# Performance work log

Hardware: AMD Instinct MI355X
Metric: run time of the kernel (lower is better)

## Reference

```python
import jax, jax.numpy as jnp
import numpy as np

ALPHA = 0.2  # LeakyReLU negative slope
NEG_BIG = -9e15


def setup_inputs() -> dict:
    key = jax.random.key(0)
    k1, k2, k3, k4 = jax.random.split(key, 4)
    N, F_IN, F_OUT = 8192, 256, 128
    h = jax.random.normal(k1, (N, F_IN), dtype=jnp.float32)
    adj = jax.random.randint(k2, (N, N), 0, 2, dtype=jnp.int32)
    # xavier_uniform with gain=1.414
    def xavier(k, shape, gain=1.414):
        fan_in, fan_out = shape[0], shape[1]
        bound = gain * np.sqrt(6.0 / (fan_in + fan_out))
        return jax.random.uniform(k, shape, jnp.float32, -bound, bound)
    W = xavier(k3, (F_IN, F_OUT))
    a = xavier(k4, (2 * F_OUT, 1))
    return {"h": h, "adj": adj, "W": W, "a": a}


def reference(h, adj, W, a):
    # Wh: [N, F_out]
    Wh = h @ W
    F_out = W.shape[1]
    a1 = a[:F_out, 0]   # attends to source (row) node
    a2 = a[F_out:, 0]   # attends to target (col) node
    # Additive decomposition of concat([Wh_i, Wh_j]) @ a:
    # e[i, j] = leaky_relu(Wh_i . a1 + Wh_j . a2)
    f1 = Wh @ a1  # [N]
    f2 = Wh @ a2  # [N]
    e = jax.nn.leaky_relu(f1[:, None] + f2[None, :], negative_slope=ALPHA)  # [N, N]
    scores = jnp.where(adj > 0, e, jnp.float32(NEG_BIG))
    attention = jax.nn.softmax(scores, axis=1)
    # dropout is identity in eval mode (training=False)
    h_prime = attention @ Wh  # [N, F_out]
    return h_prime
```

## Files before the change

kernel.cpp:

```cpp
#include <hip/hip_runtime.h>


#define N_NODES 8192
#define F_IN 256
#define F_OUT 128
#define RPB 16
#define JCH 128
#define JSPLIT 4
#define JRANGE (N_NODES / JSPLIT)
#define NCH (JRANGE / JCH)

typedef _Float16 half8 __attribute__((ext_vector_type(8)));
typedef float floatx4 __attribute__((ext_vector_type(4)));
typedef float f32x4 __attribute__((ext_vector_type(4)));

__device__ __align__(16) float g_Wh[N_NODES * F_OUT];
__device__ __align__(16) _Float16 g_WhT[(size_t)F_OUT * N_NODES];
__device__ __align__(16) float g_f1[N_NODES];
__device__ __align__(16) float g_f2[N_NODES];
__device__ __align__(16) float g_part[JSPLIT][N_NODES * F_OUT];
__device__ __align__(16) float g_spart[JSPLIT][N_NODES];

#define GLD16NT(lds, gp)                                                      \
  __builtin_amdgcn_global_load_lds(                                           \
      (const __attribute__((address_space(1))) unsigned int*)(gp),            \
      (__attribute__((address_space(3))) unsigned int*)(lds), 16, 0, 2)

__global__ __launch_bounds__(256, 2) void wh_kernel(
    const float* __restrict__ h, const float* __restrict__ W) {
  __shared__ float hT[F_IN][20];
  const int t = threadIdx.x;
  const int i0 = blockIdx.x * 16;
  {
    const int row = t >> 4;
    const int fu = t & 15;
#pragma unroll
    for (int r = 0; r < 4; ++r) {
      const int ku = r * 16 + fu;
      const float4 v = *(const float4*)(h + (size_t)(i0 + row) * F_IN + ku * 4);
      hT[ku * 4 + 0][row] = v.x; hT[ku * 4 + 1][row] = v.y;
      hT[ku * 4 + 2][row] = v.z; hT[ku * 4 + 3][row] = v.w;
    }
  }
  __syncthreads();
  const int c = t & 127;
  const int rg = t >> 7;
  float acc[8];
#pragma unroll
  for (int r = 0; r < 8; ++r) acc[r] = 0.f;
#pragma unroll 8
  for (int k = 0; k < F_IN; ++k) {
    const float wv = W[k * F_OUT + c];
    const float4 x0 = *(const float4*)(&hT[k][rg * 8]);
    const float4 x1 = *(const float4*)(&hT[k][rg * 8 + 4]);
    acc[0] = fmaf(x0.x, wv, acc[0]); acc[1] = fmaf(x0.y, wv, acc[1]);
    acc[2] = fmaf(x0.z, wv, acc[2]); acc[3] = fmaf(x0.w, wv, acc[3]);
    acc[4] = fmaf(x1.x, wv, acc[4]); acc[5] = fmaf(x1.y, wv, acc[5]);
    acc[6] = fmaf(x1.z, wv, acc[6]); acc[7] = fmaf(x1.w, wv, acc[7]);
  }
#pragma unroll
  for (int r = 0; r < 8; ++r)
    g_Wh[(size_t)(i0 + rg * 8 + r) * F_OUT + c] = acc[r];
  union { _Float16 hh[8]; uint4 u4; } pk;
#pragma unroll
  for (int r = 0; r < 8; ++r) pk.hh[r] = (_Float16)acc[r];
  *(uint4*)(g_WhT + (size_t)c * N_NODES + i0 + rg * 8) = pk.u4;
}

__global__ __launch_bounds__(256) void f12_kernel(const float* __restrict__ a) {
  const int t = threadIdx.x;
  const int row = blockIdx.x * 2 + (t >> 7);
  const int c = t & 127;
  const float wh = g_Wh[(size_t)row * F_OUT + c];
  float p1 = wh * a[c];
  float p2 = wh * a[F_OUT + c];
  for (int o = 32; o > 0; o >>= 1) {
    p1 += __shfl_down(p1, o, 64);
    p2 += __shfl_down(p2, o, 64);
  }
  __shared__ float s1[4], s2[4];
  const int w = t >> 6;
  if ((t & 63) == 0) { s1[w] = p1; s2[w] = p2; }
  __syncthreads();
  if ((t & 127) == 0) {
    g_f1[row] = s1[w] + s1[w + 1];
    g_f2[row] = s2[w] + s2[w + 1];
  }
}

__device__ __forceinline__ float score_p(int a, float f2v, float f1r) {
  float s = f1r + f2v;
  s = fmaxf(s, 0.2f * s);
  float arg = (a > 0) ? fmaf(s, 1.44269504088896f, -16.0f) : -1.0e5f;
  return __builtin_amdgcn_exp2f(arg);
}

__global__ __launch_bounds__(256, 4) void gat_attn_kernel(const int* __restrict__ adj) {
  const int t = threadIdx.x;
  const int wave = t >> 6;
  const int lane = t & 63;
  const int mrow = lane & 15;
  const int quad = lane >> 4;
  const int i0 = blockIdx.x * RPB;
  const int js = blockIdx.y;
  const int jbase = js * JRANGE;

  __shared__ int ldsAdj[2][RPB * JCH];
  __shared__ float ldsO[RPB][F_OUT];
  __shared__ float ldsS[4][RPB];

  int rm[4], cm[4];
  {
    half8 a1f, b1f, a2f, b2f;
#pragma unroll
    for (int e = 0; e < 8; ++e) {
      a1f[e] = (_Float16)0; b1f[e] = (_Float16)0;
      a2f[e] = (_Float16)0; b2f[e] = (_Float16)0;
    }
    if (quad == 0) {
      a1f[0] = (_Float16)mrow; b1f[0] = (_Float16)1;
      a2f[0] = (_Float16)1;    b2f[0] = (_Float16)mrow;
    }
    floatx4 d1 = (floatx4)0.f, d2 = (floatx4)0.f;
    d1 = __builtin_amdgcn_mfma_f32_16x16x32_f16(a1f, b1f, d1, 0, 0, 0);
    d2 = __builtin_amdgcn_mfma_f32_16x16x32_f16(a2f, b2f, d2, 0, 0, 0);
#pragma unroll
    for (int r = 0; r < 4; ++r) { rm[r] = (int)d1[r]; cm[r] = (int)d2[r]; }
  }

  const float f1r = g_f1[i0 + mrow];

  half8 ones;
#pragma unroll
  for (int e = 0; e < 8; ++e) ones[e] = (_Float16)1;

  floatx4 acc[8];
  floatx4 asum = (floatx4)0.f;
#pragma unroll
  for (int ct = 0; ct < 8; ++ct) acc[ct] = (floatx4)0.f;

#define DMA(cc, bb) do {                                                      \
    _Pragma("unroll")                                                         \
    for (int R = 0; R < 2; ++R) {                                             \
      const int m0 = wave * 4 + R * 2;                                        \
      const int m = m0 + (lane >> 5);                                         \
      const int u = ((lane & 31) - m) & 31;                                   \
      const int* gp = adj + (size_t)(i0 + m) * N_NODES + jbase + (cc) * JCH + u * 4; \
      GLD16NT(&ldsAdj[bb][m0 * JCH], gp);                                     \
    }                                                                         \
  } while (0)

  DMA(0, 0);
  __syncthreads();

  const int jloc = wave * 32 + quad * 8;
  const int u0 = jloc >> 2;

#pragma unroll 1
  for (int c = 0; c < NCH; ++c) {
    const int b = c & 1;
    const int jglob = jbase + c * JCH + jloc;

    half8 bfr[8];
#pragma unroll
    for (int ct = 0; ct < 8; ++ct)
      bfr[ct] = *(const half8*)(g_WhT + (size_t)(ct * 16 + mrow) * N_NODES + jglob);
    const float4 F0 = *(const float4*)(g_f2 + jglob);
    const float4 F1 = *(const float4*)(g_f2 + jglob + 4);

    if (c + 1 < NCH) DMA(c + 1, b ^ 1);

    const char* base = (const char*)&ldsAdj[b][0];
    const int4 A0 = *(const int4*)(base + mrow * 512 + (((u0 + mrow) & 31) << 4));
    const int4 A1 = *(const int4*)(base + mrow * 512 + (((u0 + 1 + mrow) & 31) << 4));

    half8 af;
    af[0] = (_Float16)score_p(A0.x, F0.x, f1r);
    af[1] = (_Float16)score_p(A0.y, F0.y, f1r);
    af[2] = (_Float16)score_p(A0.z, F0.z, f1r);
    af[3] = (_Float16)score_p(A0.w, F0.w, f1r);
    af[4] = (_Float16)score_p(A1.x, F1.x, f1r);
    af[5] = (_Float16)score_p(A1.y, F1.y, f1r);
    af[6] = (_Float16)score_p(A1.z, F1.z, f1r);
    af[7] = (_Float16)score_p(A1.w, F1.w, f1r);

#pragma unroll
    for (int ct = 0; ct < 8; ++ct)
      acc[ct] = __builtin_amdgcn_mfma_f32_16x16x32_f16(af, bfr[ct], acc[ct], 0, 0, 0);
    asum = __builtin_amdgcn_mfma_f32_16x16x32_f16(af, ones, asum, 0, 0, 0);

    __syncthreads();
  }
#undef DMA

  if (mrow == 0) {
#pragma unroll
    for (int r = 0; r < 4; ++r) ldsS[wave][rm[r]] = asum[r];
  }
  for (int w = 0; w < 4; ++w) {
    if (wave == w) {
#pragma unroll
      for (int ct = 0; ct < 8; ++ct)
#pragma unroll
        for (int r = 0; r < 4; ++r) {
          float* p = &ldsO[rm[r]][ct * 16 + cm[r]];
          if (w == 0) *p = acc[ct][r];
          else        *p += acc[ct][r];
        }
    }
    __syncthreads();
  }
  {
    const int row = t >> 4;
    const int c0 = (t & 15) * 8;
    float* dst = g_part[js] + (size_t)(i0 + row) * F_OUT + c0;
    *(f32x4*)(dst + 0) = *(const f32x4*)(&ldsO[row][c0 + 0]);
    *(f32x4*)(dst + 4) = *(const f32x4*)(&ldsO[row][c0 + 4]);
    if (t < RPB)
      g_spart[js][i0 + t] = ldsS[0][t] + ldsS[1][t] + ldsS[2][t] + ldsS[3][t];
  }
}

__global__ __launch_bounds__(256) void comb_kernel(float* __restrict__ out) {
  const int u = blockIdx.x * 256 + threadIdx.x;
  const int row = u >> 5;
  const float s = g_spart[0][row] + g_spart[1][row] +
                  g_spart[2][row] + g_spart[3][row];
  const f32x4 v = ((const f32x4*)g_part[0])[u] + ((const f32x4*)g_part[1])[u] +
                  ((const f32x4*)g_part[2])[u] + ((const f32x4*)g_part[3])[u];
  ((f32x4*)out)[u] = v * (1.0f / s);
}

extern "C" void kernel_launch(void* const* d_in, const int* in_sizes, int n_in,
                              void* d_out, int out_size, void* d_ws, size_t ws_size,
                              hipStream_t stream) {
  const float* h = (const float*)d_in[0];
  const int* adj = (const int*)d_in[1];
  const float* W = (const float*)d_in[2];
  const float* a = (const float*)d_in[3];
  float* out = (float*)d_out;
  (void)d_ws; (void)ws_size;

  wh_kernel<<<dim3(N_NODES / 16), dim3(256), 0, stream>>>(h, W);
  f12_kernel<<<dim3(N_NODES / 2), dim3(256), 0, stream>>>(a);
  gat_attn_kernel<<<dim3(N_NODES / RPB, JSPLIT), dim3(256), 0, stream>>>(adj);
  comb_kernel<<<dim3(N_NODES * F_OUT / 4 / 256), dim3(256), 0, stream>>>(out);
}
```

Before: 477.6 us.

## Process 64 rows per block and load adjacency directly into registers

Result: faster. 435.5 us (-8.8%).

```diff
diff --git a/kernel.cpp b/kernel.cpp
--- a/kernel.cpp
+++ b/kernel.cpp
@@ -4,7 +4,7 @@
 #define N_NODES 8192
 #define F_IN 256
 #define F_OUT 128
-#define RPB 16
+#define RPB 64
 #define JCH 128
 #define JSPLIT 4
 #define JRANGE (N_NODES / JSPLIT)
@@ -13,6 +13,7 @@
 typedef _Float16 half8 __attribute__((ext_vector_type(8)));
 typedef float floatx4 __attribute__((ext_vector_type(4)));
 typedef float f32x4 __attribute__((ext_vector_type(4)));
+typedef int i32x4 __attribute__((ext_vector_type(4)));
 
 __device__ __align__(16) float g_Wh[N_NODES * F_OUT];
 __device__ __align__(16) _Float16 g_WhT[(size_t)F_OUT * N_NODES];
@@ -20,11 +21,6 @@
 __device__ __align__(16) float g_f2[N_NODES];
 __device__ __align__(16) float g_part[JSPLIT][N_NODES * F_OUT];
 __device__ __align__(16) float g_spart[JSPLIT][N_NODES];
-
-#define GLD16NT(lds, gp)                                                      \
-  __builtin_amdgcn_global_load_lds(                                           \
-      (const __attribute__((address_space(1))) unsigned int*)(gp),            \
-      (__attribute__((address_space(3))) unsigned int*)(lds), 16, 0, 2)
 
 __global__ __launch_bounds__(256, 2) void wh_kernel(
     const float* __restrict__ h, const float* __restrict__ W) {
@@ -95,7 +91,7 @@
   return __builtin_amdgcn_exp2f(arg);
 }
 
-__global__ __launch_bounds__(256, 4) void gat_attn_kernel(const int* __restrict__ adj) {
+__global__ __launch_bounds__(256, 2) void gat_attn_kernel(const int* __restrict__ adj) {
   const int t = threadIdx.x;
   const int wave = t >> 6;
   const int lane = t & 63;
@@ -104,61 +100,27 @@
   const int i0 = blockIdx.x * RPB;
   const int js = blockIdx.y;
   const int jbase = js * JRANGE;
-
-  __shared__ int ldsAdj[2][RPB * JCH];
-  __shared__ float ldsO[RPB][F_OUT];
-  __shared__ float ldsS[4][RPB];
-
-  int rm[4], cm[4];
-  {
-    half8 a1f, b1f, a2f, b2f;
-#pragma unroll
-    for (int e = 0; e < 8; ++e) {
-      a1f[e] = (_Float16)0; b1f[e] = (_Float16)0;
-      a2f[e] = (_Float16)0; b2f[e] = (_Float16)0;
-    }
-    if (quad == 0) {
-      a1f[0] = (_Float16)mrow; b1f[0] = (_Float16)1;
-      a2f[0] = (_Float16)1;    b2f[0] = (_Float16)mrow;
-    }
-    floatx4 d1 = (floatx4)0.f, d2 = (floatx4)0.f;
-    d1 = __builtin_amdgcn_mfma_f32_16x16x32_f16(a1f, b1f, d1, 0, 0, 0);
-    d2 = __builtin_amdgcn_mfma_f32_16x16x32_f16(a2f, b2f, d2, 0, 0, 0);
-#pragma unroll
-    for (int r = 0; r < 4; ++r) { rm[r] = (int)d1[r]; cm[r] = (int)d2[r]; }
-  }
-
-  const float f1r = g_f1[i0 + mrow];
+  const int jloc = wave * 32 + quad * 8;
+
+  float f1r[4];
+#pragma unroll
+  for (int tl = 0; tl < 4; ++tl) f1r[tl] = g_f1[i0 + tl * 16 + mrow];
 
   half8 ones;
 #pragma unroll
   for (int e = 0; e < 8; ++e) ones[e] = (_Float16)1;
 
-  floatx4 acc[8];
-  floatx4 asum = (floatx4)0.f;
-#pragma unroll
-  for (int ct = 0; ct < 8; ++ct) acc[ct] = (floatx4)0.f;
-
-#define DMA(cc, bb) do {                                                      \
-    _Pragma("unroll")                                                         \
-    for (int R = 0; R < 2; ++R) {                                             \
-      const int m0 = wave * 4 + R * 2;                                        \
-      const int m = m0 + (lane >> 5);                                         \
-      const int u = ((lane & 31) - m) & 31;                                   \
-      const int* gp = adj + (size_t)(i0 + m) * N_NODES + jbase + (cc) * JCH + u * 4; \
-      GLD16NT(&ldsAdj[bb][m0 * JCH], gp);                                     \
-    }                                                                         \
-  } while (0)
-
-  DMA(0, 0);
-  __syncthreads();
-
-  const int jloc = wave * 32 + quad * 8;
-  const int u0 = jloc >> 2;
+  floatx4 acc[4][8];
+  floatx4 asum[4];
+#pragma unroll
+  for (int tl = 0; tl < 4; ++tl) {
+    asum[tl] = (floatx4)0.f;
+#pragma unroll
+    for (int ct = 0; ct < 8; ++ct) acc[tl][ct] = (floatx4)0.f;
+  }
 
 #pragma unroll 1
   for (int c = 0; c < NCH; ++c) {
-    const int b = c & 1;
     const int jglob = jbase + c * JCH + jloc;
 
     half8 bfr[8];
@@ -167,67 +129,80 @@
       bfr[ct] = *(const half8*)(g_WhT + (size_t)(ct * 16 + mrow) * N_NODES + jglob);
     const float4 F0 = *(const float4*)(g_f2 + jglob);
     const float4 F1 = *(const float4*)(g_f2 + jglob + 4);
-
-    if (c + 1 < NCH) DMA(c + 1, b ^ 1);
-
-    const char* base = (const char*)&ldsAdj[b][0];
-    const int4 A0 = *(const int4*)(base + mrow * 512 + (((u0 + mrow) & 31) << 4));
-    const int4 A1 = *(const int4*)(base + mrow * 512 + (((u0 + 1 + mrow) & 31) << 4));
-
-    half8 af;
-    af[0] = (_Float16)score_p(A0.x, F0.x, f1r);
-    af[1] = (_Float16)score_p(A0.y, F0.y, f1r);
-    af[2] = (_Float16)score_p(A0.z, F0.z, f1r);
-    af[3] = (_Float16)score_p(A0.w, F0.w, f1r);
-    af[4] = (_Float16)score_p(A1.x, F1.x, f1r);
-    af[5] = (_Float16)score_p(A1.y, F1.y, f1r);
-    af[6] = (_Float16)score_p(A1.z, F1.z, f1r);
-    af[7] = (_Float16)score_p(A1.w, F1.w, f1r);
-
-#pragma unroll
-    for (int ct = 0; ct < 8; ++ct)
-      acc[ct] = __builtin_amdgcn_mfma_f32_16x16x32_f16(af, bfr[ct], acc[ct], 0, 0, 0);
-    asum = __builtin_amdgcn_mfma_f32_16x16x32_f16(af, ones, asum, 0, 0, 0);
-
-    __syncthreads();
-  }
-#undef DMA
+    i32x4 A0[4], A1[4];
+#pragma unroll
+    for (int tl = 0; tl < 4; ++tl) {
+      const int* ap = adj + (size_t)(i0 + tl * 16 + mrow) * N_NODES + jglob;
+      A0[tl] = __builtin_nontemporal_load((const i32x4*)ap);
+      A1[tl] = __builtin_nontemporal_load((const i32x4*)ap + 1);
+    }
+
+#pragma unroll
+    for (int tl = 0; tl < 4; ++tl) {
+      half8 af;
+      af[0] = (_Float16)score_p(A0[tl][0], F0.x, f1r[tl]);
+      af[1] = (_Float16)score_p(A0[tl][1], F0.y, f1r[tl]);
+      af[2] = (_Float16)score_p(A0[tl][2], F0.z, f1r[tl]);
+      af[3] = (_Float16)score_p(A0[tl][3], F0.w, f1r[tl]);
+      af[4] = (_Float16)score_p(A1[tl][0], F1.x, f1r[tl]);
+      af[5] = (_Float16)score_p(A1[tl][1], F1.y, f1r[tl]);
+      af[6] = (_Float16)score_p(A1[tl][2], F1.z, f1r[tl]);
+      af[7] = (_Float16)score_p(A1[tl][3], F1.w, f1r[tl]);
+#pragma unroll
+      for (int ct = 0; ct < 8; ++ct)
+        acc[tl][ct] = __builtin_amdgcn_mfma_f32_16x16x32_f16(af, bfr[ct], acc[tl][ct], 0, 0, 0);
+      asum[tl] = __builtin_amdgcn_mfma_f32_16x16x32_f16(af, ones, asum[tl], 0, 0, 0);
+    }
+  }
+
+  __shared__ float ldsO[RPB][F_OUT];
+  __shared__ float ldsS[4][RPB];
 
   if (mrow == 0) {
 #pragma unroll
-    for (int r = 0; r < 4; ++r) ldsS[wave][rm[r]] = asum[r];
+    for (int tl = 0; tl < 4; ++tl)
+#pragma unroll
+      for (int r = 0; r < 4; ++r)
+        ldsS[wave][tl * 16 + quad * 4 + r] = asum[tl][r];
   }
   for (int w = 0; w < 4; ++w) {
     if (wave == w) {
 #pragma unroll
-      for (int ct = 0; ct < 8; ++ct)
-#pragma unroll
-        for (int r = 0; r < 4; ++r) {
-          float* p = &ldsO[rm[r]][ct * 16 + cm[r]];
-          if (w == 0) *p = acc[ct][r];
-          else        *p += acc[ct][r];
-        }
+      for (int tl = 0; tl < 4; ++tl)
+#pragma unroll
+        for (int ct = 0; ct < 8; ++ct)
+#pragma unroll
+          for (int r = 0; r < 4; ++r) {
+            float* p = &ldsO[tl * 16 + quad * 4 + r][ct * 16 + mrow];
+            if (w == 0) *p = acc[tl][ct][r];
+            else        *p += acc[tl][ct][r];
+          }
     }
     __syncthreads();
   }
   {
-    const int row = t >> 4;
-    const int c0 = (t & 15) * 8;
+    const int row = t >> 2;
+    const int c0 = (t & 3) * 32;
     float* dst = g_part[js] + (size_t)(i0 + row) * F_OUT + c0;
-    *(f32x4*)(dst + 0) = *(const f32x4*)(&ldsO[row][c0 + 0]);
-    *(f32x4*)(dst + 4) = *(const f32x4*)(&ldsO[row][c0 + 4]);
-    if (t < RPB)
-      g_spart[js][i0 + t] = ldsS[0][t] + ldsS[1][t] + ldsS[2][t] + ldsS[3][t];
+#pragma unroll
+    for (int q = 0; q < 8; ++q)
+      *(f32x4*)(dst + q * 4) = *(const f32x4*)(&ldsO[row][c0 + q * 4]);
+    if ((t & 3) == 0)
+      g_spart[js][i0 + row] = ldsS[0][row] + ldsS[1][row] +
+                              ldsS[2][row] + ldsS[3][row];
   }
 }
 
 __global__ __launch_bounds__(256) void comb_kernel(float* __restrict__ out) {
   const int u = blockIdx.x * 256 + threadIdx.x;
   const int row = u >> 5;
-  const float s = g_spart[0][row] + g_spart[1][row] +
-                  g_spart[2][row] + g_spart[3][row];
-  const f32x4 v = ((const f32x4*)g_part[0])[u] + ((const f32x4*)g_part[1])[u] +
-                  ((const f32x4*)g_part[2])[u] + ((const f32x4*)g_part[3])[u];
+  float s = 0.f;
+  f32x4 v = (f32x4)0.f;
+#pragma unroll
+  for (int p = 0; p < JSPLIT; ++p) {
+    s += g_spart[p][row];
+    v += ((const f32x4*)g_part[p])[u];
+  }
   ((f32x4*)out)[u] = v * (1.0f / s);
 }
 
```
